# Kernel optimization log

Measured on AMD Instinct MI355X. Metric: run time of the kernel, lower is better.

## Reference

```python
import jax, jax.numpy as jnp
import numpy as np

N_NODES = 100000
N_EDGES = 1600000
IN_FEATS = 512
OUT_FEATS = 128


def setup_inputs() -> dict:
    key = jax.random.key(0)
    k1, k2, k3, k4, k5 = jax.random.split(key, 5)
    feat = jax.random.normal(k1, (N_NODES, IN_FEATS), dtype=jnp.float32)
    src = jax.random.randint(k2, (N_EDGES,), 0, N_NODES, dtype=jnp.int32)
    dst = jax.random.randint(k3, (N_EDGES,), 0, N_NODES, dtype=jnp.int32)
    edge_weight = jax.random.uniform(k4, (N_EDGES,), dtype=jnp.float32)
    # xavier_uniform init for the [in, out] weight
    limit = float(np.sqrt(6.0 / (IN_FEATS + OUT_FEATS)))
    weight = jax.random.uniform(k5, (IN_FEATS, OUT_FEATS), dtype=jnp.float32,
                                minval=-limit, maxval=limit)
    bias = jnp.zeros((OUT_FEATS,), dtype=jnp.float32)
    return {"feat": feat, "weight": weight, "bias": bias,
            "edge_weight": edge_weight, "src": src, "dst": dst}


def reference(feat, weight, bias, edge_weight, src, dst):
    n = feat.shape[0]
    ones = jnp.ones_like(edge_weight)
    # degrees from edge list; clamp(min=1)
    out_deg = jnp.maximum(jax.ops.segment_sum(ones, src, num_segments=n), 1.0)
    in_deg = jnp.maximum(jax.ops.segment_sum(ones, dst, num_segments=n), 1.0)
    # norm='both': left-normalize source feats by out_deg^-0.5
    feat_src = feat * jax.lax.rsqrt(out_deg)[:, None]
    # in_feats > out_feats -> project before aggregation
    h = feat_src @ weight                      # [N, OUT]
    msg = h[src] * edge_weight[:, None]        # u_mul_e, [E, OUT]
    rst = jax.ops.segment_sum(msg, dst, num_segments=n)  # fn.sum per dst
    # right-normalize by in_deg^-0.5, add bias (activation is None)
    rst = rst * jax.lax.rsqrt(in_deg)[:, None] + bias
    return rst
```

## Files before the change

kernel.cpp:

```cpp
#include <hip/hip_runtime.h>
#include <hip/hip_bf16.h>

#define NNODES 100000
#define NEDGES 1600000
#define INF 512
#define OUTF 128
#define NB 391
#define BCAP 5120
#define SEG 2048
#define BK 32
#define NKSTEP (INF / BK)

typedef __attribute__((ext_vector_type(8))) __bf16 bf16x8;
typedef __attribute__((ext_vector_type(4))) float f32x4;
typedef __attribute__((ext_vector_type(2))) float f32x2;

typedef const __attribute__((address_space(1))) unsigned int* gas_ptr;
typedef __attribute__((address_space(3))) unsigned int* las_ptr;

__device__ __forceinline__ void gload_lds16(const void* g, void* l) {
  __builtin_amdgcn_global_load_lds((gas_ptr)g, (las_ptr)l, 16, 0, 0);
}

__global__ void wt_kernel(const float* __restrict__ w, unsigned short* __restrict__ wta) {
  int i = blockIdx.x * blockDim.x + threadIdx.x;
  if (i >= 8192) return;
  int lane = i & 63;
  int c8   = (i >> 6) & 7;
  int kb   = i >> 9;
  int n = c8 * 16 + (lane & 15);
  int kbase = kb * 32 + (lane >> 4) * 8;
  unsigned short tmp[8];
#pragma unroll
  for (int j = 0; j < 8; ++j) {
    __bf16 b = (__bf16)(w[(size_t)(kbase + j) * OUTF + n]);
    tmp[j] = __builtin_bit_cast(unsigned short, b);
  }
  ((int4*)wta)[i] = *(int4*)tmp;
}

__global__ __launch_bounds__(256) void bucket_kernel(
    const int* __restrict__ src, const int* __restrict__ dst,
    const float* __restrict__ ew, int* __restrict__ out_cnt,
    int* __restrict__ bucket_cnt, int2* __restrict__ bucket) {
  __shared__ int hist[NB];
  __shared__ int base[NB];
  int t = threadIdx.x;
  for (int i = t; i < NB; i += 256) hist[i] = 0;
  __syncthreads();
  int e0 = blockIdx.x * SEG;
  int e1 = min(e0 + SEG, NEDGES);
  for (int e = e0 + t; e < e1; e += 256) {
    atomicAdd(&out_cnt[src[e]], 1);
    atomicAdd(&hist[dst[e] >> 8], 1);
  }
  __syncthreads();
  for (int i = t; i < NB; i += 256) {
    int c = hist[i];
    base[i] = c ? atomicAdd(&bucket_cnt[i], c) : 0;
    hist[i] = 0;
  }
  __syncthreads();
  for (int e = e0 + t; e < e1; e += 256) {
    int d = dst[e];
    int b = d >> 8;
    int r = atomicAdd(&hist[b], 1);
    int2 en;
    en.x = ((d & 255) << 17) | src[e];
    en.y = __float_as_int(ew[e]);
    bucket[(size_t)b * BCAP + base[b] + r] = en;
  }
}

__global__ __launch_bounds__(512) void bscan_kernel(const int* __restrict__ bucket_cnt,
                                                    int* __restrict__ bucket_base,
                                                    int* __restrict__ rowptr) {
  __shared__ int s[512];
  int t = threadIdx.x;
  int v = (t < NB) ? bucket_cnt[t] : 0;
  s[t] = v;
  __syncthreads();
  for (int off = 1; off < 512; off <<= 1) {
    int x = (t >= off) ? s[t - off] : 0;
    __syncthreads();
    s[t] += x;
    __syncthreads();
  }
  if (t < NB) bucket_base[t] = s[t] - v;
  if (t == 0) rowptr[NNODES] = NEDGES;
}

__global__ __launch_bounds__(256) void csr_kernel(
    const int* __restrict__ bucket_cnt, const int* __restrict__ bucket_base,
    const int2* __restrict__ bucket, int* __restrict__ rowptr,
    int2* __restrict__ epair) {
  __shared__ int hist[256];
  __shared__ int cur[256];
  int b = blockIdx.x;
  int t = threadIdx.x;
  int nb = bucket_cnt[b];
  int bbase = bucket_base[b];
  const int2* bk = bucket + (size_t)b * BCAP;
  hist[t] = 0;
  __syncthreads();
  for (int i = t; i < nb; i += 256) atomicAdd(&hist[bk[i].x >> 17], 1);
  __syncthreads();
  int v = hist[t];
  for (int off = 1; off < 256; off <<= 1) {
    int x = (t >= off) ? hist[t - off] : 0;
    __syncthreads();
    hist[t] += x;
    __syncthreads();
  }
  int excl = hist[t] - v;
  int node = b * 256 + t;
  if (node < NNODES) rowptr[node] = bbase + excl;
  cur[t] = excl;
  __syncthreads();
  for (int i = t; i < nb; i += 256) {
    int2 en = bk[i];
    int nl = en.x >> 17;
    int r = atomicAdd(&cur[nl], 1);
    epair[bbase + r] = make_int2(en.x & 0x1FFFF, en.y);
  }
}

__global__ __launch_bounds__(256, 4) void gemm_kernel(
    const float* __restrict__ feat, const unsigned short* __restrict__ wta,
    const int* __restrict__ out_cnt, unsigned short* __restrict__ h) {
  __shared__ float As[2][64 * BK];
  __shared__ unsigned short Bs[2][4096];

  const int t = threadIdx.x;
  const int lane = t & 63;
  const int wave = t >> 6;
  const int l15 = lane & 15;
  const int lg  = lane >> 4;
  const int rowbase = blockIdx.x * 64;

  const int srow_off = lane >> 3;
  const int schunk = (lane & 7) ^ srow_off;

  int r0 = rowbase + wave * 16 + l15;
  float s0 = rsqrtf(fmaxf((float)out_cnt[min(r0, NNODES - 1)], 1.0f));

  f32x4 acc[8];
#pragma unroll
  for (int c = 0; c < 8; ++c) acc[c] = (f32x4){0.f, 0.f, 0.f, 0.f};

#define STAGE(buf, kb)                                                         \
  {                                                                            \
    _Pragma("unroll")                                                          \
    for (int q = 0; q < 2; ++q) {                                              \
      int i = wave * 2 + q;                                                    \
      int gr = min(rowbase + i * 8 + srow_off, NNODES - 1);                    \
      const float* ga = feat + (size_t)gr * INF + (kb) * BK + schunk * 4;      \
      gload_lds16(ga, &As[buf][i * 256]);                                      \
      const unsigned short* gb =                                               \
          wta + (size_t)(kb) * 4096 + i * 512 + lane * 8;                      \
      gload_lds16(gb, &Bs[buf][i * 512]);                                      \
    }                                                                          \
  }

  int buf = 0;
  STAGE(0, 0);
  __syncthreads();

  for (int kb = 0; kb < NKSTEP; ++kb) {
    if (kb + 1 < NKSTEP) STAGE(buf ^ 1, kb + 1);

    bf16x8 bfr[8];
#pragma unroll
    for (int c = 0; c < 8; ++c)
      bfr[c] = *(const bf16x8*)&Bs[buf][c * 512 + lane * 8];

    int r = wave * 16 + l15;
    int c0 = (lg * 2) ^ (l15 & 7);
    int c1 = (lg * 2 + 1) ^ (l15 & 7);
    f32x4 u = *(const f32x4*)&As[buf][r * 32 + c0 * 4];
    f32x4 v = *(const f32x4*)&As[buf][r * 32 + c1 * 4];
    bf16x8 a;
#pragma unroll
    for (int j = 0; j < 4; ++j) {
      a[j]     = (__bf16)(u[j] * s0);
      a[j + 4] = (__bf16)(v[j] * s0);
    }

#pragma unroll
    for (int c = 0; c < 8; ++c)
      acc[c] = __builtin_amdgcn_mfma_f32_16x16x32_bf16(a, bfr[c], acc[c], 0, 0, 0);

    __syncthreads();
    buf ^= 1;
  }
#undef STAGE

  int rb = rowbase + wave * 16 + lg * 4;
#pragma unroll
  for (int r = 0; r < 4; ++r) {
    int row = rb + r;
    if (row < NNODES) {
#pragma unroll
      for (int c = 0; c < 8; ++c) {
        __bf16 bv = (__bf16)acc[c][r];
        h[(size_t)row * OUTF + c * 16 + l15] = __builtin_bit_cast(unsigned short, bv);
      }
    }
  }
}

__device__ __forceinline__ float blo(unsigned int u) { return __uint_as_float(u << 16); }
__device__ __forceinline__ float bhi(unsigned int u) { return __uint_as_float(u & 0xFFFF0000u); }

__global__ __launch_bounds__(256) void gather_kernel(
    const int* __restrict__ rowptr, const int2* __restrict__ epair,
    const unsigned short* __restrict__ h, const float* __restrict__ bias,
    float* __restrict__ out) {
  const int lane = threadIdx.x & 63;
  const int half = lane >> 5;
  const int grp  = (lane >> 4) & 1;
  const int li   = lane & 15;
  const int wid  = (blockIdx.x * blockDim.x + threadIdx.x) >> 6;
  const int nw   = (gridDim.x * blockDim.x) >> 6;

  for (int p = wid; p < NNODES / 2; p += nw) {
    const int node = p * 2 + half;
    const int beg = rowptr[node];
    const int end = rowptr[node + 1];

    float a0 = 0.f, a1 = 0.f, a2 = 0.f, a3 = 0.f;
    float a4 = 0.f, a5 = 0.f, a6 = 0.f, a7 = 0.f;

    int e = beg + grp;
#define GSTEP(pr)                                                              \
      {                                                                        \
        const unsigned int* hp =                                               \
            (const unsigned int*)(h + (size_t)(pr).x * OUTF) + li * 4;         \
        uint4 u = *(const uint4*)hp;                                           \
        float w = __int_as_float((pr).y);                                      \
        a0 += blo(u.x) * w; a1 += bhi(u.x) * w;                                \
        a2 += blo(u.y) * w; a3 += bhi(u.y) * w;                                \
        a4 += blo(u.z) * w; a5 += bhi(u.z) * w;                                \
        a6 += blo(u.w) * w; a7 += bhi(u.w) * w;                                \
      }
    for (; e + 6 < end; e += 8) {
      int2 p0 = epair[e];
      int2 p1 = epair[e + 2];
      int2 p2 = epair[e + 4];
      int2 p3 = epair[e + 6];
      GSTEP(p0); GSTEP(p1); GSTEP(p2); GSTEP(p3);
    }
    for (; e < end; e += 2) {
      int2 pr = epair[e];
      GSTEP(pr);
    }
#undef GSTEP

    a0 += __shfl_xor(a0, 16); a1 += __shfl_xor(a1, 16);
    a2 += __shfl_xor(a2, 16); a3 += __shfl_xor(a3, 16);
    a4 += __shfl_xor(a4, 16); a5 += __shfl_xor(a5, 16);
    a6 += __shfl_xor(a6, 16); a7 += __shfl_xor(a7, 16);

    if (grp == 0) {
      float sc = rsqrtf(fmaxf((float)(end - beg), 1.0f));
      f32x4 b0 = ((const f32x4*)bias)[li * 2];
      f32x4 b1 = ((const f32x4*)bias)[li * 2 + 1];
      f32x4 v0, v1;
      v0.x = a0 * sc + b0.x; v0.y = a1 * sc + b0.y;
      v0.z = a2 * sc + b0.z; v0.w = a3 * sc + b0.w;
      v1.x = a4 * sc + b1.x; v1.y = a5 * sc + b1.y;
      v1.z = a6 * sc + b1.z; v1.w = a7 * sc + b1.w;
      f32x4* op = (f32x4*)(out + (size_t)node * OUTF);
      op[li * 2] = v0;
      op[li * 2 + 1] = v1;
    }
  }
}

extern "C" void kernel_launch(void* const* d_in, const int* in_sizes, int n_in,
                              void* d_out, int out_size, void* d_ws, size_t ws_size,
                              hipStream_t stream) {
  const float* feat   = (const float*)d_in[0];
  const float* weight = (const float*)d_in[1];
  const float* bias   = (const float*)d_in[2];
  const float* ew     = (const float*)d_in[3];
  const int*   src    = (const int*)d_in[4];
  const int*   dst    = (const int*)d_in[5];
  float* out = (float*)d_out;
  char* ws = (char*)d_ws;

  int* out_cnt        = (int*)ws;
  int* rowptr         = (int*)(ws + 0x80000);
  int* bucket_cnt     = (int*)(ws + 0x100000);
  int* bucket_base    = (int*)(ws + 0x101000);
  unsigned short* wta = (unsigned short*)(ws + 0x110000);
  int2* bucket        = (int2*)(ws + 0x140000);
  int2* epair         = (int2*)(ws + 0x1200000);
  unsigned short* h   = (unsigned short*)(ws + 0x2000000);

  hipMemsetAsync(out_cnt, 0, NNODES * sizeof(int), stream);
  hipMemsetAsync(bucket_cnt, 0, NB * sizeof(int), stream);

  wt_kernel<<<32, 256, 0, stream>>>(weight, wta);
  bucket_kernel<<<(NEDGES + SEG - 1) / SEG, 256, 0, stream>>>(src, dst, ew, out_cnt,
                                                              bucket_cnt, bucket);
  bscan_kernel<<<1, 512, 0, stream>>>(bucket_cnt, bucket_base, rowptr);
  csr_kernel<<<NB, 256, 0, stream>>>(bucket_cnt, bucket_base, bucket, rowptr, epair);
  gemm_kernel<<<(NNODES + 63) / 64, 256, 0, stream>>>(feat, wta, out_cnt, h);
  gather_kernel<<<2048, 256, 0, stream>>>(rowptr, epair, h, bias, out);
}
```

Baseline: 251.7 us.

## Fuse edge bucketing with GEMM and CSR build with aggregation

Bucketing and the GEMM now run as separate block ranges of one launch so they can overlap. The per-bucket CSR sort is folded into the aggregation kernel, which keeps row offsets in shared memory and drops the global scan and the rowptr array. The out-degree normalization moves from scaling the GEMM input rows to scaling each edge weight, which removes the GEMM's dependence on the degree counts. In exchange, aggregation now runs only 391 blocks of 512 threads, which may limit parallelism in the gather phase.

```diff
diff --git a/kernel.cpp b/kernel.cpp
--- a/kernel.cpp
+++ b/kernel.cpp
@@ -8,12 +8,13 @@
 #define NB 391
 #define BCAP 5120
 #define SEG 2048
+#define NBUCKBLK ((NEDGES + SEG - 1) / SEG)
+#define NGEMMBLK ((NNODES + 63) / 64)
 #define BK 32
 #define NKSTEP (INF / BK)
 
 typedef __attribute__((ext_vector_type(8))) __bf16 bf16x8;
 typedef __attribute__((ext_vector_type(4))) float f32x4;
-typedef __attribute__((ext_vector_type(2))) float f32x2;
 
 typedef const __attribute__((address_space(1))) unsigned int* gas_ptr;
 typedef __attribute__((address_space(3))) unsigned int* las_ptr;
@@ -39,110 +40,57 @@
   ((int4*)wta)[i] = *(int4*)tmp;
 }
 
-__global__ __launch_bounds__(256) void bucket_kernel(
+struct GemmSmem { float As[2][64 * BK]; unsigned short Bs[2][4096]; };
+struct BuckSmem { int hist[NB]; int base[NB]; };
+union FusedSmem { GemmSmem g; BuckSmem bu; };
+
+__global__ __launch_bounds__(256, 4) void fused_kernel(
+    const float* __restrict__ feat, const unsigned short* __restrict__ wta,
     const int* __restrict__ src, const int* __restrict__ dst,
     const float* __restrict__ ew, int* __restrict__ out_cnt,
-    int* __restrict__ bucket_cnt, int2* __restrict__ bucket) {
-  __shared__ int hist[NB];
-  __shared__ int base[NB];
-  int t = threadIdx.x;
-  for (int i = t; i < NB; i += 256) hist[i] = 0;
-  __syncthreads();
-  int e0 = blockIdx.x * SEG;
-  int e1 = min(e0 + SEG, NEDGES);
-  for (int e = e0 + t; e < e1; e += 256) {
-    atomicAdd(&out_cnt[src[e]], 1);
-    atomicAdd(&hist[dst[e] >> 8], 1);
-  }
-  __syncthreads();
-  for (int i = t; i < NB; i += 256) {
-    int c = hist[i];
-    base[i] = c ? atomicAdd(&bucket_cnt[i], c) : 0;
-    hist[i] = 0;
-  }
-  __syncthreads();
-  for (int e = e0 + t; e < e1; e += 256) {
-    int d = dst[e];
-    int b = d >> 8;
-    int r = atomicAdd(&hist[b], 1);
-    int2 en;
-    en.x = ((d & 255) << 17) | src[e];
-    en.y = __float_as_int(ew[e]);
-    bucket[(size_t)b * BCAP + base[b] + r] = en;
-  }
-}
-
-__global__ __launch_bounds__(512) void bscan_kernel(const int* __restrict__ bucket_cnt,
-                                                    int* __restrict__ bucket_base,
-                                                    int* __restrict__ rowptr) {
-  __shared__ int s[512];
-  int t = threadIdx.x;
-  int v = (t < NB) ? bucket_cnt[t] : 0;
-  s[t] = v;
-  __syncthreads();
-  for (int off = 1; off < 512; off <<= 1) {
-    int x = (t >= off) ? s[t - off] : 0;
-    __syncthreads();
-    s[t] += x;
-    __syncthreads();
-  }
-  if (t < NB) bucket_base[t] = s[t] - v;
-  if (t == 0) rowptr[NNODES] = NEDGES;
-}
-
-__global__ __launch_bounds__(256) void csr_kernel(
-    const int* __restrict__ bucket_cnt, const int* __restrict__ bucket_base,
-    const int2* __restrict__ bucket, int* __restrict__ rowptr,
-    int2* __restrict__ epair) {
-  __shared__ int hist[256];
-  __shared__ int cur[256];
-  int b = blockIdx.x;
-  int t = threadIdx.x;
-  int nb = bucket_cnt[b];
-  int bbase = bucket_base[b];
-  const int2* bk = bucket + (size_t)b * BCAP;
-  hist[t] = 0;
-  __syncthreads();
-  for (int i = t; i < nb; i += 256) atomicAdd(&hist[bk[i].x >> 17], 1);
-  __syncthreads();
-  int v = hist[t];
-  for (int off = 1; off < 256; off <<= 1) {
-    int x = (t >= off) ? hist[t - off] : 0;
-    __syncthreads();
-    hist[t] += x;
-    __syncthreads();
-  }
-  int excl = hist[t] - v;
-  int node = b * 256 + t;
-  if (node < NNODES) rowptr[node] = bbase + excl;
-  cur[t] = excl;
-  __syncthreads();
-  for (int i = t; i < nb; i += 256) {
-    int2 en = bk[i];
-    int nl = en.x >> 17;
-    int r = atomicAdd(&cur[nl], 1);
-    epair[bbase + r] = make_int2(en.x & 0x1FFFF, en.y);
-  }
-}
-
-__global__ __launch_bounds__(256, 4) void gemm_kernel(
-    const float* __restrict__ feat, const unsigned short* __restrict__ wta,
-    const int* __restrict__ out_cnt, unsigned short* __restrict__ h) {
-  __shared__ float As[2][64 * BK];
-  __shared__ unsigned short Bs[2][4096];
-
+    int* __restrict__ bucket_cnt, int2* __restrict__ bucket,
+    unsigned short* __restrict__ h) {
+  __shared__ FusedSmem sm;
   const int t = threadIdx.x;
+
+  if (blockIdx.x < NBUCKBLK) {
+    int* hist = sm.bu.hist;
+    int* base = sm.bu.base;
+    for (int i = t; i < NB; i += 256) hist[i] = 0;
+    __syncthreads();
+    int e0 = blockIdx.x * SEG;
+    int e1 = min(e0 + SEG, NEDGES);
+    for (int e = e0 + t; e < e1; e += 256) {
+      atomicAdd(&out_cnt[src[e]], 1);
+      atomicAdd(&hist[dst[e] >> 8], 1);
+    }
+    __syncthreads();
+    for (int i = t; i < NB; i += 256) {
+      int c = hist[i];
+      base[i] = c ? atomicAdd(&bucket_cnt[i], c) : 0;
+      hist[i] = 0;
+    }
+    __syncthreads();
+    for (int e = e0 + t; e < e1; e += 256) {
+      int d = dst[e];
+      int b = d >> 8;
+      int r = atomicAdd(&hist[b], 1);
+      int2 en;
+      en.x = ((d & 255) << 17) | src[e];
+      en.y = __float_as_int(ew[e]);
+      bucket[(size_t)b * BCAP + base[b] + r] = en;
+    }
+    return;
+  }
+
   const int lane = t & 63;
   const int wave = t >> 6;
   const int l15 = lane & 15;
   const int lg  = lane >> 4;
-  const int rowbase = blockIdx.x * 64;
+  const int rowbase = (blockIdx.x - NBUCKBLK) * 64;
 
   const int srow_off = lane >> 3;
   const int schunk = (lane & 7) ^ srow_off;
-
-  int r0 = rowbase + wave * 16 + l15;
-  float s0 = rsqrtf(fmaxf((float)out_cnt[min(r0, NNODES - 1)], 1.0f));
 
   f32x4 acc[8];
 #pragma unroll
@@ -155,10 +103,10 @@
       int i = wave * 2 + q;                                                    \
       int gr = min(rowbase + i * 8 + srow_off, NNODES - 1);                    \
       const float* ga = feat + (size_t)gr * INF + (kb) * BK + schunk * 4;      \
-      gload_lds16(ga, &As[buf][i * 256]);                                      \
+      gload_lds16(ga, &sm.g.As[buf][i * 256]);                                 \
       const unsigned short* gb =                                               \
           wta + (size_t)(kb) * 4096 + i * 512 + lane * 8;                      \
-      gload_lds16(gb, &Bs[buf][i * 512]);                                      \
+      gload_lds16(gb, &sm.g.Bs[buf][i * 512]);                                 \
     }                                                                          \
   }
 
@@ -172,18 +120,18 @@
     bf16x8 bfr[8];
 #pragma unroll
     for (int c = 0; c < 8; ++c)
-      bfr[c] = *(const bf16x8*)&Bs[buf][c * 512 + lane * 8];
+      bfr[c] = *(const bf16x8*)&sm.g.Bs[buf][c * 512 + lane * 8];
 
     int r = wave * 16 + l15;
     int c0 = (lg * 2) ^ (l15 & 7);
     int c1 = (lg * 2 + 1) ^ (l15 & 7);
-    f32x4 u = *(const f32x4*)&As[buf][r * 32 + c0 * 4];
-    f32x4 v = *(const f32x4*)&As[buf][r * 32 + c1 * 4];
+    f32x4 u = *(const f32x4*)&sm.g.As[buf][r * 32 + c0 * 4];
+    f32x4 v = *(const f32x4*)&sm.g.As[buf][r * 32 + c1 * 4];
     bf16x8 a;
 #pragma unroll
     for (int j = 0; j < 4; ++j) {
-      a[j]     = (__bf16)(u[j] * s0);
-      a[j + 4] = (__bf16)(v[j] * s0);
+      a[j]     = (__bf16)u[j];
+      a[j + 4] = (__bf16)v[j];
     }
 
 #pragma unroll
@@ -212,21 +160,62 @@
 __device__ __forceinline__ float blo(unsigned int u) { return __uint_as_float(u << 16); }
 __device__ __forceinline__ float bhi(unsigned int u) { return __uint_as_float(u & 0xFFFF0000u); }
 
-__global__ __launch_bounds__(256) void gather_kernel(
-    const int* __restrict__ rowptr, const int2* __restrict__ epair,
+__global__ __launch_bounds__(512) void agg_kernel(
+    const int* __restrict__ bucket_cnt, const int2* __restrict__ bucket,
+    const int* __restrict__ out_cnt, int2* __restrict__ epair,
     const unsigned short* __restrict__ h, const float* __restrict__ bias,
     float* __restrict__ out) {
-  const int lane = threadIdx.x & 63;
+  __shared__ int hist[256];
+  __shared__ int rowp[256];
+  __shared__ int cur[256];
+  __shared__ int dcnt[256];
+  const int b = blockIdx.x;
+  const int t = threadIdx.x;
+  const int nb = bucket_cnt[b];
+  const int2* bk = bucket + (size_t)b * BCAP;
+  int2* ep = epair + (size_t)b * BCAP;
+
+  if (t < 256) hist[t] = 0;
+  __syncthreads();
+  for (int i = t; i < nb; i += 512) atomicAdd(&hist[bk[i].x >> 17], 1);
+  __syncthreads();
+  int myv = (t < 256) ? hist[t] : 0;
+  __syncthreads();
+  for (int off = 1; off < 256; off <<= 1) {
+    int x = (t < 256 && t >= off) ? hist[t - off] : 0;
+    __syncthreads();
+    if (t < 256) hist[t] += x;
+    __syncthreads();
+  }
+  if (t < 256) {
+    int excl = hist[t] - myv;
+    rowp[t] = excl;
+    cur[t] = excl;
+    dcnt[t] = myv;
+  }
+  __syncthreads();
+  for (int i = t; i < nb; i += 512) {
+    int2 en = bk[i];
+    int s = en.x & 0x1FFFF;
+    int nl = en.x >> 17;
+    float w = __int_as_float(en.y) * rsqrtf(fmaxf((float)out_cnt[s], 1.0f));
+    int r = atomicAdd(&cur[nl], 1);
+    ep[r] = make_int2(s, __float_as_int(w));
+  }
+  __syncthreads();
+
+  const int lane = t & 63;
+  const int wv = t >> 6;
   const int half = lane >> 5;
   const int grp  = (lane >> 4) & 1;
   const int li   = lane & 15;
-  const int wid  = (blockIdx.x * blockDim.x + threadIdx.x) >> 6;
-  const int nw   = (gridDim.x * blockDim.x) >> 6;
-
-  for (int p = wid; p < NNODES / 2; p += nw) {
-    const int node = p * 2 + half;
-    const int beg = rowptr[node];
-    const int end = rowptr[node + 1];
+
+  for (int pi = wv; pi < 128; pi += 8) {
+    const int nl = pi * 2 + half;
+    const int node = b * 256 + nl;
+    const int beg = rowp[nl];
+    const int deg = dcnt[nl];
+    const int endp = beg + deg;
 
     float a0 = 0.f, a1 = 0.f, a2 = 0.f, a3 = 0.f;
     float a4 = 0.f, a5 = 0.f, a6 = 0.f, a7 = 0.f;
@@ -243,15 +232,15 @@
         a4 += blo(u.z) * w; a5 += bhi(u.z) * w;                                \
         a6 += blo(u.w) * w; a7 += bhi(u.w) * w;                                \
       }
-    for (; e + 6 < end; e += 8) {
-      int2 p0 = epair[e];
-      int2 p1 = epair[e + 2];
-      int2 p2 = epair[e + 4];
-      int2 p3 = epair[e + 6];
+    for (; e + 6 < endp; e += 8) {
+      int2 p0 = ep[e];
+      int2 p1 = ep[e + 2];
+      int2 p2 = ep[e + 4];
+      int2 p3 = ep[e + 6];
       GSTEP(p0); GSTEP(p1); GSTEP(p2); GSTEP(p3);
     }
-    for (; e < end; e += 2) {
-      int2 pr = epair[e];
+    for (; e < endp; e += 2) {
+      int2 pr = ep[e];
       GSTEP(pr);
     }
 #undef GSTEP
@@ -261,8 +250,8 @@
     a4 += __shfl_xor(a4, 16); a5 += __shfl_xor(a5, 16);
     a6 += __shfl_xor(a6, 16); a7 += __shfl_xor(a7, 16);
 
-    if (grp == 0) {
-      float sc = rsqrtf(fmaxf((float)(end - beg), 1.0f));
+    if (grp == 0 && node < NNODES) {
+      float sc = rsqrtf(fmaxf((float)deg, 1.0f));
       f32x4 b0 = ((const f32x4*)bias)[li * 2];
       f32x4 b1 = ((const f32x4*)bias)[li * 2 + 1];
       f32x4 v0, v1;
@@ -290,22 +279,17 @@
   char* ws = (char*)d_ws;
 
   int* out_cnt        = (int*)ws;
-  int* rowptr         = (int*)(ws + 0x80000);
   int* bucket_cnt     = (int*)(ws + 0x100000);
-  int* bucket_base    = (int*)(ws + 0x101000);
   unsigned short* wta = (unsigned short*)(ws + 0x110000);
   int2* bucket        = (int2*)(ws + 0x140000);
   int2* epair         = (int2*)(ws + 0x1200000);
-  unsigned short* h   = (unsigned short*)(ws + 0x2000000);
+  unsigned short* h   = (unsigned short*)(ws + 0x2200000);
 
   hipMemsetAsync(out_cnt, 0, NNODES * sizeof(int), stream);
   hipMemsetAsync(bucket_cnt, 0, NB * sizeof(int), stream);
 
   wt_kernel<<<32, 256, 0, stream>>>(weight, wta);
-  bucket_kernel<<<(NEDGES + SEG - 1) / SEG, 256, 0, stream>>>(src, dst, ew, out_cnt,
-                                                              bucket_cnt, bucket);
-  bscan_kernel<<<1, 512, 0, stream>>>(bucket_cnt, bucket_base, rowptr);
-  csr_kernel<<<NB, 256, 0, stream>>>(bucket_cnt, bucket_base, bucket, rowptr, epair);
-  gemm_kernel<<<(NNODES + 63) / 64, 256, 0, stream>>>(feat, wta, out_cnt, h);
-  gather_kernel<<<2048, 256, 0, stream>>>(rowptr, epair, h, bias, out);
-}
+  fused_kernel<<<NBUCKBLK + NGEMMBLK, 256, 0, stream>>>(feat, wta, src, dst, ew,
+                                                        out_cnt, bucket_cnt, bucket, h);
+  agg_kernel<<<NB, 512, 0, stream>>>(bucket_cnt, bucket, out_cnt, epair, h, bias, out);
+}
```

Result: slower. 270.2 us (+7.3%).

## Drop LDS staging in GEMM; load A and B fragments directly from global

Applied to the files above, without the earlier changes.

The GEMM kernel no longer stages feat and weight tiles through shared memory with global_load_lds and block barriers. Each lane now reads its own A fragment from global memory, software-pipelined two k-steps ahead in registers, and reads its B fragments straight from the pre-swizzled weight buffer, which stays hot in cache. This removes the LDS traffic and the per-step __syncthreads, and occupancy bounds drop from 4 to 3 to leave room for the extra registers. The trade-offs are uncoalesced-looking strided per-row loads of feat and repeated global/L2 reads of the weight fragments by every wave.

```diff
diff --git a/kernel.cpp b/kernel.cpp
--- a/kernel.cpp
+++ b/kernel.cpp
@@ -14,13 +14,6 @@
 typedef __attribute__((ext_vector_type(8))) __bf16 bf16x8;
 typedef __attribute__((ext_vector_type(4))) float f32x4;
 typedef __attribute__((ext_vector_type(2))) float f32x2;
-
-typedef const __attribute__((address_space(1))) unsigned int* gas_ptr;
-typedef __attribute__((address_space(3))) unsigned int* las_ptr;
-
-__device__ __forceinline__ void gload_lds16(const void* g, void* l) {
-  __builtin_amdgcn_global_load_lds((gas_ptr)g, (las_ptr)l, 16, 0, 0);
-}
 
 __global__ void wt_kernel(const float* __restrict__ w, unsigned short* __restrict__ wta) {
   int i = blockIdx.x * blockDim.x + threadIdx.x;
@@ -125,60 +118,43 @@
   }
 }
 
-__global__ __launch_bounds__(256, 4) void gemm_kernel(
+__global__ __launch_bounds__(256, 3) void gemm_kernel(
     const float* __restrict__ feat, const unsigned short* __restrict__ wta,
     const int* __restrict__ out_cnt, unsigned short* __restrict__ h) {
-  __shared__ float As[2][64 * BK];
-  __shared__ unsigned short Bs[2][4096];
-
-  const int t = threadIdx.x;
-  const int lane = t & 63;
-  const int wave = t >> 6;
+  const int lane = threadIdx.x & 63;
+  const int wave = threadIdx.x >> 6;
   const int l15 = lane & 15;
   const int lg  = lane >> 4;
   const int rowbase = blockIdx.x * 64;
 
-  const int srow_off = lane >> 3;
-  const int schunk = (lane & 7) ^ srow_off;
-
-  int r0 = rowbase + wave * 16 + l15;
-  float s0 = rsqrtf(fmaxf((float)out_cnt[min(r0, NNODES - 1)], 1.0f));
+  const int row = min(rowbase + wave * 16 + l15, NNODES - 1);
+  const float s0 = rsqrtf(fmaxf((float)out_cnt[row], 1.0f));
+  const float* fp = feat + (size_t)row * INF + lg * 8;
 
   f32x4 acc[8];
 #pragma unroll
   for (int c = 0; c < 8; ++c) acc[c] = (f32x4){0.f, 0.f, 0.f, 0.f};
 
-#define STAGE(buf, kb)                                                         \
-  {                                                                            \
-    _Pragma("unroll")                                                          \
-    for (int q = 0; q < 2; ++q) {                                              \
-      int i = wave * 2 + q;                                                    \
-      int gr = min(rowbase + i * 8 + srow_off, NNODES - 1);                    \
-      const float* ga = feat + (size_t)gr * INF + (kb) * BK + schunk * 4;      \
-      gload_lds16(ga, &As[buf][i * 256]);                                      \
-      const unsigned short* gb =                                               \
-          wta + (size_t)(kb) * 4096 + i * 512 + lane * 8;                      \
-      gload_lds16(gb, &Bs[buf][i * 512]);                                      \
-    }                                                                          \
-  }
-
-  int buf = 0;
-  STAGE(0, 0);
-  __syncthreads();
-
+  f32x4 ua[2], va[2];
+  ua[0] = *(const f32x4*)(fp + 0);
+  va[0] = *(const f32x4*)(fp + 4);
+  ua[1] = *(const f32x4*)(fp + BK);
+  va[1] = *(const f32x4*)(fp + BK + 4);
+
+#pragma unroll
   for (int kb = 0; kb < NKSTEP; ++kb) {
-    if (kb + 1 < NKSTEP) STAGE(buf ^ 1, kb + 1);
+    f32x4 u = ua[kb & 1];
+    f32x4 v = va[kb & 1];
+    if (kb + 2 < NKSTEP) {
+      ua[kb & 1] = *(const f32x4*)(fp + (kb + 2) * BK);
+      va[kb & 1] = *(const f32x4*)(fp + (kb + 2) * BK + 4);
+    }
 
     bf16x8 bfr[8];
 #pragma unroll
     for (int c = 0; c < 8; ++c)
-      bfr[c] = *(const bf16x8*)&Bs[buf][c * 512 + lane * 8];
-
-    int r = wave * 16 + l15;
-    int c0 = (lg * 2) ^ (l15 & 7);
-    int c1 = (lg * 2 + 1) ^ (l15 & 7);
-    f32x4 u = *(const f32x4*)&As[buf][r * 32 + c0 * 4];
-    f32x4 v = *(const f32x4*)&As[buf][r * 32 + c1 * 4];
+      bfr[c] = *(const bf16x8*)(wta + (size_t)kb * 4096 + c * 512 + lane * 8);
+
     bf16x8 a;
 #pragma unroll
     for (int j = 0; j < 4; ++j) {
@@ -189,21 +165,17 @@
 #pragma unroll
     for (int c = 0; c < 8; ++c)
       acc[c] = __builtin_amdgcn_mfma_f32_16x16x32_bf16(a, bfr[c], acc[c], 0, 0, 0);
-
-    __syncthreads();
-    buf ^= 1;
-  }
-#undef STAGE
+  }
 
   int rb = rowbase + wave * 16 + lg * 4;
 #pragma unroll
   for (int r = 0; r < 4; ++r) {
-    int row = rb + r;
-    if (row < NNODES) {
+    int orow = rb + r;
+    if (orow < NNODES) {
 #pragma unroll
       for (int c = 0; c < 8; ++c) {
         __bf16 bv = (__bf16)acc[c][r];
-        h[(size_t)row * OUTF + c * 16 + l15] = __builtin_bit_cast(unsigned short, bv);
+        h[(size_t)orow * OUTF + c * 16 + l15] = __builtin_bit_cast(unsigned short, bv);
       }
     }
   }
```

Result: slower. 282.0 us (+12.0%).
